# Optimization experiments

Measured on AMD Instinct MI355X. Metric: run time of the kernel, lower is better.

## Reference

```python
import jax, jax.numpy as jnp
import numpy as np

B, C, V, L = 32, 32, 1024, 13  # batch, channels, nodes, seq_len
SUPPORT_LEN, ORDER = 3, 2
C_IN_TOTAL = (ORDER * SUPPORT_LEN + 1) * C  # 224
C_OUT = 64


def setup_inputs() -> dict:
    key = jax.random.key(0)
    ks = jax.random.split(key, 6)
    x = jax.random.normal(ks[0], (B, C, V, L), dtype=jnp.float32)
    # row-normalized random adjacencies (dense diffusion matrices)
    def adj(k):
        a = jax.random.uniform(k, (V, V), dtype=jnp.float32)
        return a / jnp.sum(a, axis=1, keepdims=True)
    A0, A1, A2 = adj(ks[1]), adj(ks[2]), adj(ks[3])
    W = jax.random.normal(ks[4], (C_OUT, C_IN_TOTAL), dtype=jnp.float32) * (1.0 / np.sqrt(C_IN_TOTAL))
    b = jnp.zeros((C_OUT,), dtype=jnp.float32)
    return {"x": x, "A0": A0, "A1": A1, "A2": A2, "W": W, "b": b}


def nconv(x, A):
    # x: [b, c, v, l], A: [v, w] -> [b, c, w, l]
    return jnp.einsum('bcvl,vw->bcwl', x, A)


def reference(x, A0, A1, A2, W, b):
    out = [x]
    for A in (A0, A1, A2):
        x1 = nconv(x, A)
        out.append(x1)
        for _ in range(2, ORDER + 1):
            x2 = nconv(x1, A)
            out.append(x2)
            x1 = x2
    h = jnp.concatenate(out, axis=1)  # [b, (order*support_len+1)*c, v, l]
    # 1x1 conv == channel contraction; dropout is identity in eval mode
    return jnp.einsum('bcvl,oc->bovl', h, W) + b[None, :, None, None]
```

## Files before the change

kernel.cpp:

```cpp
#include <hip/hip_runtime.h>
#include <hip/hip_bf16.h>
#include <cstdint>


#define SZE 13631488ull
#define OFF_AT  190840832ull
#define OFF_WB  197132288ull
#define WS_NEED 197160960ull

typedef __attribute__((ext_vector_type(8))) short short8;
typedef __attribute__((ext_vector_type(4))) float f32x4;

__device__ __forceinline__ unsigned short f2b(float f) {
    unsigned int u = __builtin_bit_cast(unsigned int, f);
    u += 0x7FFFu + ((u >> 16) & 1u);
    return (unsigned short)(u >> 16);
}

__device__ __forceinline__ void gl2lds16(const unsigned short* g, unsigned short* l) {
    __builtin_amdgcn_global_load_lds(
        (__attribute__((address_space(1))) void*)(g),
        (__attribute__((address_space(3))) void*)(l), 16, 0, 0);
}

__global__ __launch_bounds__(256) void k_prep(const float* __restrict__ x,
                                              unsigned short* __restrict__ T,
                                              unsigned short* __restrict__ Ht) {
    __shared__ unsigned short sb[32 * 840];
    const int b = blockIdx.x >> 4, vc = blockIdx.x & 15;
    const int t = threadIdx.x;
    const float4* xb = (const float4*)x;
    for (int it = 0; it < 26; ++it) {
        int q = it * 256 + t;
        int c = q / 208, f = q - c * 208;
        float4 u = xb[(size_t)(b * 32 + c) * 3328 + vc * 208 + f];
        ushort4 pk; pk.x = f2b(u.x); pk.y = f2b(u.y); pk.z = f2b(u.z); pk.w = f2b(u.w);
        *(ushort4*)(sb + c * 840 + f * 4) = pk;
    }
    __syncthreads();
    unsigned short* Tb = T + (size_t)b * 13 * 32 * 1024 + (size_t)vc * 64;
    for (int it = 0; it < 26; ++it) {
        int q = it * 256 + t;
        int l = q >> 9, r = q & 511, c = r >> 4, sg = r & 15;
        const unsigned short* src = sb + c * 840 + l;
        ushort4 pk;
        pk.x = src[(sg * 4 + 0) * 13];
        pk.y = src[(sg * 4 + 1) * 13];
        pk.z = src[(sg * 4 + 2) * 13];
        pk.w = src[(sg * 4 + 3) * 13];
        *(ushort4*)(Tb + (size_t)(l * 32 + c) * 1024 + sg * 4) = pk;
    }
    unsigned short* Hb = Ht + ((size_t)b * 13312 + (size_t)vc * 832) * 224;
    for (int it = 0; it < 26; ++it) {
        int q = it * 256 + t;
        int v = q / 104, r = q - v * 104, l = r >> 3, cs = r & 7;
        const unsigned short* src = sb + v * 13 + l;
        ushort4 pk;
        pk.x = src[(cs * 4 + 0) * 840];
        pk.y = src[(cs * 4 + 1) * 840];
        pk.z = src[(cs * 4 + 2) * 840];
        pk.w = src[(cs * 4 + 3) * 840];
        *(ushort4*)(Hb + (size_t)(v * 13 + l) * 224 + cs * 4) = pk;
    }
}

__global__ __launch_bounds__(256) void k_prep_A(const float* __restrict__ A0,
                                                const float* __restrict__ A1,
                                                const float* __restrict__ A2,
                                                unsigned short* __restrict__ AT) {
    const float* A = blockIdx.z == 0 ? A0 : blockIdx.z == 1 ? A1 : A2;
    unsigned short* D = AT + (size_t)blockIdx.z * 1024 * 1024;
    __shared__ float tile[32][33];
    int v0 = blockIdx.y * 32, w0 = blockIdx.x * 32;
    int c = threadIdx.x & 31, r = threadIdx.x >> 5;
    for (int p = 0; p < 4; ++p) {
        int rr = r + p * 8;
        tile[rr][c] = A[(size_t)(v0 + rr) * 1024 + w0 + c];
    }
    __syncthreads();
    for (int p = 0; p < 4; ++p) {
        int rr = r + p * 8;
        D[(size_t)(w0 + rr) * 1024 + v0 + c] = f2b(tile[c][rr]);
    }
}

__global__ __launch_bounds__(256) void k_prep_W(const float* __restrict__ W,
                                                unsigned short* __restrict__ Wb) {
    int idx = blockIdx.x * 256 + threadIdx.x;
    Wb[idx] = f2b(W[idx]);
}

__global__ __launch_bounds__(256) void k_gemm(const unsigned short* __restrict__ Xb, long xz,
                                              const unsigned short* __restrict__ Pb,
                                              unsigned short* __restrict__ Tout, long tz,
                                              unsigned short* __restrict__ Ht, int cc0b,
                                              int doT) {
    __shared__ union {
        struct { unsigned short xs[8192]; unsigned short ps[8192]; } s;
        unsigned short cs[128 * 132];
        unsigned short ct[128 * 136];
    } lds;
    const int z = blockIdx.z;
    const unsigned short* X = Xb + (size_t)z * (size_t)xz;
    const unsigned short* P = Pb + (size_t)z * (1024u * 1024u);
    const int i0 = blockIdx.x * 128;
    const int j0 = blockIdx.y * 128;
    const int t = threadIdx.x;
    const int lane = t & 63, wave = t >> 6;
    const int l16 = lane & 15, quad = lane >> 4;
    const int wi = (wave >> 1) * 64, wj = (wave & 1) * 64;

    f32x4 acc[4][4] = {};

    const int row = t >> 2, seg = t & 3;
    const unsigned short* xg0 = X + (size_t)(i0 + row) * 1024 + seg * 8;
    const unsigned short* xg1 = xg0 + (size_t)64 * 1024;
    const unsigned short* pg0 = P + (size_t)(j0 + row) * 1024 + seg * 8;
    const unsigned short* pg1 = pg0 + (size_t)64 * 1024;
    unsigned short* lx0 = lds.s.xs + t * 8;
    unsigned short* lp0 = lds.s.ps + t * 8;

    for (int kt = 0; kt < 16; ++kt) {
        const int ko = kt * 64;
        gl2lds16(xg0 + ko,      lx0);
        gl2lds16(xg1 + ko,      lx0 + 2048);
        gl2lds16(xg0 + ko + 32, lx0 + 4096);
        gl2lds16(xg1 + ko + 32, lx0 + 6144);
        gl2lds16(pg0 + ko,      lp0);
        gl2lds16(pg1 + ko,      lp0 + 2048);
        gl2lds16(pg0 + ko + 32, lp0 + 4096);
        gl2lds16(pg1 + ko + 32, lp0 + 6144);
        __syncthreads();
#pragma unroll
        for (int p = 0; p < 2; ++p) {
            short8 a[4], b[4];
#pragma unroll
            for (int mi = 0; mi < 4; ++mi)
                a[mi] = *(const short8*)(lds.s.xs + p * 4096 + (wi + mi * 16 + l16) * 32 + quad * 8);
#pragma unroll
            for (int nj = 0; nj < 4; ++nj)
                b[nj] = *(const short8*)(lds.s.ps + p * 4096 + (wj + nj * 16 + l16) * 32 + quad * 8);
#pragma unroll
            for (int mi = 0; mi < 4; ++mi)
#pragma unroll
                for (int nj = 0; nj < 4; ++nj)
                    acc[mi][nj] = __builtin_amdgcn_mfma_f32_16x16x32_bf16(a[mi], b[nj], acc[mi][nj], 0, 0, 0);
        }
        __syncthreads();
    }

    if (doT) {
#pragma unroll
        for (int mi = 0; mi < 4; ++mi)
#pragma unroll
            for (int nj = 0; nj < 4; ++nj)
#pragma unroll
                for (int r = 0; r < 4; ++r)
                    lds.cs[(wi + mi * 16 + quad * 4 + r) * 132 + (wj + nj * 16 + l16)] =
                        f2b(acc[mi][nj][r]);
        __syncthreads();
        unsigned short* O = Tout + (size_t)z * (size_t)tz;
#pragma unroll
        for (int rep = 0; rep < 8; ++rep) {
            int q = rep * 256 + t;
            int rr = q >> 4, sg = q & 15;
            *(uint4*)(O + (size_t)(i0 + rr) * 1024 + j0 + sg * 8) =
                *(const uint4*)(lds.cs + rr * 132 + sg * 8);
        }
        __syncthreads();
    }

#pragma unroll
    for (int mi = 0; mi < 4; ++mi)
#pragma unroll
        for (int nj = 0; nj < 4; ++nj) {
            ushort4 pk;
            pk.x = f2b(acc[mi][nj][0]);
            pk.y = f2b(acc[mi][nj][1]);
            pk.z = f2b(acc[mi][nj][2]);
            pk.w = f2b(acc[mi][nj][3]);
            *(ushort4*)(lds.ct + (wj + nj * 16 + l16) * 136 + wi + mi * 16 + quad * 4) = pk;
        }
    __syncthreads();
    const int cc0 = cc0b + 64 * z;
#pragma unroll
    for (int it = 0; it < 8; ++it) {
        int q = it * 256 + t;
        int sg = q & 3, v = (q >> 2) & 127, s = q >> 9;
        int p = (i0 >> 5) + s;
        int b = p / 13, l = p - b * 13;
        size_t m = (size_t)b * 13312 + (size_t)(j0 + v) * 13 + l;
        *(uint4*)(Ht + m * 224 + cc0 + sg * 8) =
            *(const uint4*)(lds.ct + v * 136 + s * 32 + sg * 8);
    }
}

__global__ __launch_bounds__(256) void k_fc(const unsigned short* __restrict__ Ht,
                                            const unsigned short* __restrict__ Wb,
                                            const float* __restrict__ bias,
                                            float* __restrict__ y) {
    __shared__ union {
        struct { unsigned short w[64 * 232]; unsigned short a[208 * 32]; } s;
        float sy[64 * 212];
    } lds;
    const int bid = blockIdx.x;
    const int b = bid >> 6, v0 = (bid & 63) * 16;
    const size_t m0 = (size_t)b * 13312 + (size_t)v0 * 13;
    const int t = threadIdx.x;
    const int lane = t & 63, wave = t >> 6;
    const int l16 = lane & 15, quad = lane >> 4;
    const int o0 = wave * 16;

    for (int it = 0; it < 7; ++it) {
        int q = it * 256 + t;
        int o = q / 28, sg = q % 28;
        *(uint4*)(lds.s.w + o * 232 + sg * 8) = *(const uint4*)(Wb + o * 224 + sg * 8);
    }
    float bv = bias[o0 + l16];
    f32x4 acc[13];
#pragma unroll
    for (int mf = 0; mf < 13; ++mf) acc[mf] = (f32x4){bv, bv, bv, bv};

    for (int kk = 0; kk < 7; ++kk) {
        __syncthreads();
        for (int it = 0; it < 4; ++it) {
            int q = it * 256 + t;
            if (q < 832)
                gl2lds16(Ht + (m0 + (q >> 2)) * 224 + kk * 32 + (q & 3) * 8,
                         lds.s.a + q * 8);
        }
        __syncthreads();
        short8 bf = *(const short8*)(lds.s.w + (o0 + l16) * 232 + kk * 32 + quad * 8);
#pragma unroll
        for (int mf = 0; mf < 13; ++mf) {
            short8 af = *(const short8*)(lds.s.a + (mf * 16 + l16) * 32 + quad * 8);
            acc[mf] = __builtin_amdgcn_mfma_f32_16x16x32_bf16(af, bf, acc[mf], 0, 0, 0);
        }
    }
    __syncthreads();
#pragma unroll
    for (int mf = 0; mf < 13; ++mf)
#pragma unroll
        for (int r = 0; r < 4; ++r)
            lds.sy[(o0 + l16) * 212 + mf * 16 + quad * 4 + r] = acc[mf][r];
    __syncthreads();
    float* yb = y + (size_t)b * 851968 + (size_t)v0 * 13;
    for (int it = 0; it < 13; ++it) {
        int q = it * 256 + t;
        int o = q / 52, sg = q % 52;
        *(float4*)(yb + (size_t)o * 13312 + sg * 4) = *(const float4*)(lds.sy + o * 212 + sg * 4);
    }
}

extern "C" void kernel_launch(void* const* d_in, const int* in_sizes, int n_in,
                              void* d_out, int out_size, void* d_ws, size_t ws_size,
                              hipStream_t stream) {
    const float* x    = (const float*)d_in[0];
    const float* A0   = (const float*)d_in[1];
    const float* A1   = (const float*)d_in[2];
    const float* A2   = (const float*)d_in[3];
    const float* W    = (const float*)d_in[4];
    const float* bias = (const float*)d_in[5];

    if (ws_size < WS_NEED) return;

    unsigned short* Ht = (unsigned short*)d_ws;
    unsigned short* AT = (unsigned short*)((char*)d_ws + OFF_AT);
    unsigned short* Wb = (unsigned short*)((char*)d_ws + OFF_WB);
    unsigned short* Tarena = (unsigned short*)d_out;

    k_prep<<<512, 256, 0, stream>>>(x, Tarena, Ht);
    k_prep_A<<<dim3(32, 32, 3), 256, 0, stream>>>(A0, A1, A2, AT);
    k_prep_W<<<56, 256, 0, stream>>>(W, Wb);
    k_gemm<<<dim3(104, 8, 3), 256, 0, stream>>>(Tarena, 0L, AT,
                                                Tarena + SZE, (long)SZE, Ht, 32, 1);
    k_gemm<<<dim3(104, 8, 3), 256, 0, stream>>>(Tarena + SZE, (long)SZE, AT,
                                                nullptr, 0L, Ht, 64, 0);
    k_fc<<<2048, 256, 0, stream>>>(Ht, Wb, bias, (float*)d_out);
}
```

Measured before the change: 511.0 us.

## Load GEMM and FC operands directly from global into registers, dropping LDS staging

Both the diffusion GEMM and the final 1x1-conv kernel stop staging operands through LDS with barriers. Each lane now reads its MFMA fragments straight from global memory, with register double-buffering in the GEMM, and the FC kernel writes results directly without an LDS transpose. This removes the LDS traffic and the __syncthreads stalls. In exchange each wave re-reads tiles that were shared in LDS, which raises global and L2 traffic, and the 16-byte per-lane loads along rows with a 2KB stride are poorly coalesced.

```diff
diff --git a/kernel.cpp b/kernel.cpp
--- a/kernel.cpp
+++ b/kernel.cpp
@@ -15,12 +15,6 @@
     unsigned int u = __builtin_bit_cast(unsigned int, f);
     u += 0x7FFFu + ((u >> 16) & 1u);
     return (unsigned short)(u >> 16);
-}
-
-__device__ __forceinline__ void gl2lds16(const unsigned short* g, unsigned short* l) {
-    __builtin_amdgcn_global_load_lds(
-        (__attribute__((address_space(1))) void*)(g),
-        (__attribute__((address_space(3))) void*)(l), 16, 0, 0);
 }
 
 __global__ __launch_bounds__(256) void k_prep(const float* __restrict__ x,
@@ -96,7 +90,6 @@
                                               unsigned short* __restrict__ Ht, int cc0b,
                                               int doT) {
     __shared__ union {
-        struct { unsigned short xs[8192]; unsigned short ps[8192]; } s;
         unsigned short cs[128 * 132];
         unsigned short ct[128 * 136];
     } lds;
@@ -110,43 +103,38 @@
     const int l16 = lane & 15, quad = lane >> 4;
     const int wi = (wave >> 1) * 64, wj = (wave & 1) * 64;
 
+    const unsigned short* xr[4];
+    const unsigned short* pr[4];
+#pragma unroll
+    for (int mi = 0; mi < 4; ++mi)
+        xr[mi] = X + (size_t)(i0 + wi + mi * 16 + l16) * 1024 + quad * 8;
+#pragma unroll
+    for (int nj = 0; nj < 4; ++nj)
+        pr[nj] = P + (size_t)(j0 + wj + nj * 16 + l16) * 1024 + quad * 8;
+
     f32x4 acc[4][4] = {};
-
-    const int row = t >> 2, seg = t & 3;
-    const unsigned short* xg0 = X + (size_t)(i0 + row) * 1024 + seg * 8;
-    const unsigned short* xg1 = xg0 + (size_t)64 * 1024;
-    const unsigned short* pg0 = P + (size_t)(j0 + row) * 1024 + seg * 8;
-    const unsigned short* pg1 = pg0 + (size_t)64 * 1024;
-    unsigned short* lx0 = lds.s.xs + t * 8;
-    unsigned short* lp0 = lds.s.ps + t * 8;
-
-    for (int kt = 0; kt < 16; ++kt) {
-        const int ko = kt * 64;
-        gl2lds16(xg0 + ko,      lx0);
-        gl2lds16(xg1 + ko,      lx0 + 2048);
-        gl2lds16(xg0 + ko + 32, lx0 + 4096);
-        gl2lds16(xg1 + ko + 32, lx0 + 6144);
-        gl2lds16(pg0 + ko,      lp0);
-        gl2lds16(pg1 + ko,      lp0 + 2048);
-        gl2lds16(pg0 + ko + 32, lp0 + 4096);
-        gl2lds16(pg1 + ko + 32, lp0 + 6144);
-        __syncthreads();
-#pragma unroll
-        for (int p = 0; p < 2; ++p) {
-            short8 a[4], b[4];
-#pragma unroll
-            for (int mi = 0; mi < 4; ++mi)
-                a[mi] = *(const short8*)(lds.s.xs + p * 4096 + (wi + mi * 16 + l16) * 32 + quad * 8);
+    short8 a[2][4], b[2][4];
+#pragma unroll
+    for (int mi = 0; mi < 4; ++mi) a[0][mi] = *(const short8*)(xr[mi]);
+#pragma unroll
+    for (int nj = 0; nj < 4; ++nj) b[0][nj] = *(const short8*)(pr[nj]);
+
+#pragma unroll
+    for (int kf = 0; kf < 32; ++kf) {
+        const int cur = kf & 1, nxt = cur ^ 1;
+        if (kf < 31) {
+            const int k = (kf + 1) * 32;
+#pragma unroll
+            for (int mi = 0; mi < 4; ++mi) a[nxt][mi] = *(const short8*)(xr[mi] + k);
+#pragma unroll
+            for (int nj = 0; nj < 4; ++nj) b[nxt][nj] = *(const short8*)(pr[nj] + k);
+        }
+#pragma unroll
+        for (int mi = 0; mi < 4; ++mi)
 #pragma unroll
             for (int nj = 0; nj < 4; ++nj)
-                b[nj] = *(const short8*)(lds.s.ps + p * 4096 + (wj + nj * 16 + l16) * 32 + quad * 8);
-#pragma unroll
-            for (int mi = 0; mi < 4; ++mi)
-#pragma unroll
-                for (int nj = 0; nj < 4; ++nj)
-                    acc[mi][nj] = __builtin_amdgcn_mfma_f32_16x16x32_bf16(a[mi], b[nj], acc[mi][nj], 0, 0, 0);
-        }
-        __syncthreads();
+                acc[mi][nj] = __builtin_amdgcn_mfma_f32_16x16x32_bf16(a[cur][mi], b[cur][nj],
+                                                                      acc[mi][nj], 0, 0, 0);
     }
 
     if (doT) {
@@ -199,57 +187,34 @@
                                             const unsigned short* __restrict__ Wb,
                                             const float* __restrict__ bias,
                                             float* __restrict__ y) {
-    __shared__ union {
-        struct { unsigned short w[64 * 232]; unsigned short a[208 * 32]; } s;
-        float sy[64 * 212];
-    } lds;
     const int bid = blockIdx.x;
     const int b = bid >> 6, v0 = (bid & 63) * 16;
     const size_t m0 = (size_t)b * 13312 + (size_t)v0 * 13;
     const int t = threadIdx.x;
     const int lane = t & 63, wave = t >> 6;
     const int l16 = lane & 15, quad = lane >> 4;
-    const int o0 = wave * 16;
-
-    for (int it = 0; it < 7; ++it) {
-        int q = it * 256 + t;
-        int o = q / 28, sg = q % 28;
-        *(uint4*)(lds.s.w + o * 232 + sg * 8) = *(const uint4*)(Wb + o * 224 + sg * 8);
-    }
-    float bv = bias[o0 + l16];
+    const int oc = wave * 16 + l16;
+
+    const unsigned short* hb = Ht + (m0 + l16) * 224 + quad * 8;
+    const unsigned short* wb = Wb + (size_t)oc * 224 + quad * 8;
+    float bv = bias[oc];
     f32x4 acc[13];
 #pragma unroll
     for (int mf = 0; mf < 13; ++mf) acc[mf] = (f32x4){bv, bv, bv, bv};
 
+#pragma unroll
     for (int kk = 0; kk < 7; ++kk) {
-        __syncthreads();
-        for (int it = 0; it < 4; ++it) {
-            int q = it * 256 + t;
-            if (q < 832)
-                gl2lds16(Ht + (m0 + (q >> 2)) * 224 + kk * 32 + (q & 3) * 8,
-                         lds.s.a + q * 8);
-        }
-        __syncthreads();
-        short8 bf = *(const short8*)(lds.s.w + (o0 + l16) * 232 + kk * 32 + quad * 8);
+        short8 wf = *(const short8*)(wb + kk * 32);
 #pragma unroll
         for (int mf = 0; mf < 13; ++mf) {
-            short8 af = *(const short8*)(lds.s.a + (mf * 16 + l16) * 32 + quad * 8);
-            acc[mf] = __builtin_amdgcn_mfma_f32_16x16x32_bf16(af, bf, acc[mf], 0, 0, 0);
-        }
-    }
-    __syncthreads();
+            short8 hf = *(const short8*)(hb + (size_t)mf * 16 * 224 + kk * 32);
+            acc[mf] = __builtin_amdgcn_mfma_f32_16x16x32_bf16(hf, wf, acc[mf], 0, 0, 0);
+        }
+    }
+    float* yb = y + (size_t)b * 851968 + (size_t)oc * 13312 + (size_t)v0 * 13 + quad * 4;
 #pragma unroll
     for (int mf = 0; mf < 13; ++mf)
-#pragma unroll
-        for (int r = 0; r < 4; ++r)
-            lds.sy[(o0 + l16) * 212 + mf * 16 + quad * 4 + r] = acc[mf][r];
-    __syncthreads();
-    float* yb = y + (size_t)b * 851968 + (size_t)v0 * 13;
-    for (int it = 0; it < 13; ++it) {
-        int q = it * 256 + t;
-        int o = q / 52, sg = q % 52;
-        *(float4*)(yb + (size_t)o * 13312 + sg * 4) = *(const float4*)(lds.sy + o * 212 + sg * 4);
-    }
+        *(f32x4*)(yb + mf * 16) = acc[mf];
 }
 
 extern "C" void kernel_launch(void* const* d_in, const int* in_sizes, int n_in,
```

New measurement: 897.4 us. +75.6%, slower.
